# Kernel optimization log

Measured on AMD Instinct MI355X. Metric: run time of the kernel, lower is better.

The kernel has to match this reference:

```python
import jax
import jax.numpy as jnp
import numpy as np

ALPHA = 0.95
NUM_POS_FREQS = 4
CROSS_WEIGHT = 0.5
TOPK = 16
EPS = 1e-12


def _pos_enc(coords):
    # coords: [N, 4] -> [N, 4 * 2 * NUM_POS_FREQS]
    N = coords.shape[0]
    freqs = 2.0 ** jnp.arange(NUM_POS_FREQS, dtype=coords.dtype)  # [F]
    angles = coords[:, :, None] * (2.0 * jnp.pi) * freqs          # [N,4,F]
    pe = jnp.concatenate([jnp.sin(angles), jnp.cos(angles)], axis=-1)  # [N,4,2F]
    return pe.reshape(N, -1)


def _cosine_sim(x, y):
    # row-wise cosine similarity: [N,C] x [M,C] -> [N,M]
    xn = x / jnp.maximum(jnp.linalg.norm(x, axis=-1, keepdims=True), EPS)
    yn = y / jnp.maximum(jnp.linalg.norm(y, axis=-1, keepdims=True), EPS)
    return xn @ yn.T


def _sparsify_topk(A, k):
    # row-wise top-k, self-loop always kept (diag forced to max before top-k)
    N = A.shape[0]
    diag = jnp.arange(N)
    A_with_self = A.at[diag, diag].set(jnp.finfo(A.dtype).max)
    _, topk_idx = jax.lax.top_k(A_with_self, k)                   # [N,k]
    mask = jnp.zeros(A.shape, dtype=bool).at[diag[:, None], topk_idx].set(True)
    return jnp.where(mask, A, jnp.zeros((), A.dtype))


def _sym_normalize(A):
    deg = jnp.clip(A.sum(axis=-1, keepdims=True), EPS, None)      # [N,1]
    d_inv_sqrt = deg ** -0.5
    return d_inv_sqrt * A * d_inv_sqrt.T


def _build_adjacency(features, coordinates, history_features, history_coords):
    B, C = features.shape
    n, K, _ = history_features.shape
    H = n * K

    cur_feats = features
    cur_pos = _pos_enc(coordinates)
    A_cur = ALPHA * _cosine_sim(cur_feats, cur_feats) + (1.0 - ALPHA) * _cosine_sim(cur_pos, cur_pos)

    hist_feats = history_features.reshape(H, C)
    hist_pos = _pos_enc(history_coords.reshape(H, 4))
    A_hist = ALPHA * _cosine_sim(hist_feats, hist_feats) + (1.0 - ALPHA) * _cosine_sim(hist_pos, hist_pos)

    A_cross = ALPHA * _cosine_sim(cur_feats, hist_feats) + (1.0 - ALPHA) * _cosine_sim(cur_pos, hist_pos)
    A_cross = CROSS_WEIGHT * A_cross

    A = jnp.block([[A_cur, A_cross], [A_cross.T, A_hist]])        # [N,N], N=B+H
    node_feats = jnp.concatenate([cur_feats, hist_feats], axis=0)

    N = A.shape[0]
    if TOPK is not None and TOPK < N:
        A = _sparsify_topk(A, TOPK)
    A = _sym_normalize(A)
    return A[None], node_feats[None]


def setup_inputs() -> dict:
    key = jax.random.key(0)
    k1, k2, k3, k4 = jax.random.split(key, 4)
    B, C, n, K = 4096, 256, 128, 32
    return {
        "features": jax.random.normal(k1, (B, C), dtype=jnp.float32),
        "coordinates": jax.random.uniform(k2, (B, 4), dtype=jnp.float32),
        "history_features": jax.random.normal(k3, (n, K, C), dtype=jnp.float32),
        "history_coords": jax.random.uniform(k4, (n, K, 4), dtype=jnp.float32),
    }


def reference(features, coordinates, history_features, history_coords):
    adj, node_feats = _build_adjacency(features, coordinates, history_features, history_coords)
    return adj, node_feats
```

## Files before the change

### kernel.cpp

```cpp
#include <hip/hip_runtime.h>
#include <math.h>

#define B_CUR 4096
#define N_TOT 8192
#define C_F   256
#define C_TOT 288
#define KSEL  16
#define NTILE 64

typedef unsigned short u16;
typedef __attribute__((ext_vector_type(8))) short short8;
typedef __attribute__((ext_vector_type(4))) float floatx4;

__device__ inline float bf2f(u16 v) {
  union { unsigned int u; float f; } x; x.u = ((unsigned int)v) << 16; return x.f;
}
__device__ inline u16 f2bf(float f) {
  union { float f; unsigned int u; } x; x.f = f;
  unsigned int u = x.u;
  u += ((u >> 16) & 1u) + 0x7FFFu;
  return (u16)(u >> 16);
}

#define GLD_LDS16(g, l) __builtin_amdgcn_global_load_lds(                      \
    (const __attribute__((address_space(1))) unsigned int*)(g),                \
    (__attribute__((address_space(3))) unsigned int*)(l), 16, 0, 0)

__global__ __launch_bounds__(256) void k_prep(
    const float* __restrict__ feats, const float* __restrict__ hfeats,
    const float* __restrict__ coords, const float* __restrict__ hcoords,
    u16* __restrict__ Zb, float* __restrict__ out_nf) {
  int wave = threadIdx.x >> 6;
  int lane = threadIdx.x & 63;
  int row  = blockIdx.x * 4 + wave;
  const float* src = (row < B_CUR) ? (feats + (size_t)row * C_F)
                                   : (hfeats + (size_t)(row - B_CUR) * C_F);
  int c0 = lane * 4;
  float4 raw = *(const float4*)(src + c0);
  float ss = raw.x*raw.x + raw.y*raw.y + raw.z*raw.z + raw.w*raw.w;
  #pragma unroll
  for (int m = 32; m; m >>= 1) ss += __shfl_xor(ss, m, 64);
  float scale = 0.97467943448089633f / fmaxf(sqrtf(ss), 1e-12f);
  ushort4 o;
  o.x = f2bf(raw.x*scale); o.y = f2bf(raw.y*scale);
  o.z = f2bf(raw.z*scale); o.w = f2bf(raw.w*scale);
  *(ushort4*)(Zb + (size_t)row * C_TOT + c0) = o;
  *(float4*)(out_nf + (size_t)row * C_F + c0) = raw;

  const float* csrc = (row < B_CUR) ? (coords + (size_t)row * 4)
                                    : (hcoords + (size_t)(row - B_CUR) * 4);
  int d = lane >> 3, sc = (lane >> 2) & 1, f = lane & 3;
  float c = csrc[d & 3];
  float ang = c * 6.283185307179586f * (float)(1 << f);
  float pe = sc ? cosf(ang) : sinf(ang);
  float p2 = pe * pe;
  #pragma unroll
  for (int m = 16; m; m >>= 1) p2 += __shfl_xor(p2, m, 64);
  float pscale = 0.22360679774997896f / fmaxf(sqrtf(p2), 1e-12f);
  if (lane < 32) Zb[(size_t)row * C_TOT + C_F + lane] = f2bf(pe * pscale);
}

#define EP_STRIDE 136
__global__ __launch_bounds__(256) void k_gemm_mfma(const u16* __restrict__ Zb,
                                                   u16* __restrict__ adj16) {
  __shared__ __align__(16) u16 smem[2 * 128 * 96];
  u16* As = smem;
  u16* Bs = smem + 128 * 96;
  int tid  = threadIdx.x;

  int t = blockIdx.x;
  int bi = (int)floorf(((2.0f*NTILE + 1.0f) -
            sqrtf((float)((2*NTILE+1)*(2*NTILE+1)) - 8.0f*(float)t)) * 0.5f);
  if (bi < 0) bi = 0; if (bi > NTILE-1) bi = NTILE-1;
  while (bi > 0 && t < bi*NTILE - bi*(bi-1)/2) --bi;
  while (bi < NTILE-1 && t >= (bi+1)*NTILE - (bi+1)*bi/2) ++bi;
  int bj = bi + (t - (bi*NTILE - bi*(bi-1)/2));

  int wave = tid >> 6, lane = tid & 63;
  int quad = lane >> 4, l16 = lane & 15;
  int m0w  = (wave >> 1) * 64;
  int n0w  = (wave & 1) * 64;
  int i0   = bi * 128, j0 = bj * 128;

  floatx4 acc[4][4];
  #pragma unroll
  for (int a = 0; a < 4; ++a)
    #pragma unroll
    for (int b = 0; b < 4; ++b) acc[a][b] = (floatx4){0.f, 0.f, 0.f, 0.f};

  for (int kt = 0; kt < C_TOT; kt += 96) {
    #pragma unroll
    for (int it = 0; it < 6; ++it) {
      int s   = it * 256 + tid;
      int row = s / 12, seg = s % 12;
      const u16* ga = Zb + (size_t)(i0 + row) * C_TOT + kt + seg * 8;
      const u16* gb = Zb + (size_t)(j0 + row) * C_TOT + kt + seg * 8;
      GLD_LDS16(ga, As + s * 8);
      GLD_LDS16(gb, Bs + s * 8);
    }
    __builtin_amdgcn_s_waitcnt(0);
    __syncthreads();
    #pragma unroll
    for (int ks = 0; ks < 3; ++ks) {
      short8 af[4], bf[4];
      #pragma unroll
      for (int mi = 0; mi < 4; ++mi)
        af[mi] = *(const short8*)(&As[(m0w + mi*16 + l16) * 96 + ks*32 + quad*8]);
      #pragma unroll
      for (int ni = 0; ni < 4; ++ni)
        bf[ni] = *(const short8*)(&Bs[(n0w + ni*16 + l16) * 96 + ks*32 + quad*8]);
      #pragma unroll
      for (int mi = 0; mi < 4; ++mi)
        #pragma unroll
        for (int ni = 0; ni < 4; ++ni)
          acc[mi][ni] = __builtin_amdgcn_mfma_f32_16x16x32_bf16(
              af[mi], bf[ni], acc[mi][ni], 0, 0, 0);
    }
    __syncthreads();
  }

  float w = ((bi < 32) != (bj < 32)) ? 0.5f : 1.0f;

  #pragma unroll
  for (int mi = 0; mi < 4; ++mi) {
    #pragma unroll
    for (int ni = 0; ni < 4; ++ni) {
      int col = n0w + ni * 16 + l16;
      #pragma unroll
      for (int rg = 0; rg < 4; ++rg) {
        int row = m0w + mi * 16 + quad * 4 + rg;
        smem[row * EP_STRIDE + col] = f2bf(acc[mi][ni][rg] * w);
      }
    }
  }
  __syncthreads();
  #pragma unroll
  for (int it = 0; it < 8; ++it) {
    int idx = it * 256 + tid;
    int row = idx >> 4, l = idx & 15;
    uint4 v = *(const uint4*)(&smem[row * EP_STRIDE + l * 8]);
    *(uint4*)(&adj16[(size_t)(i0 + row) * 16384 + j0 + l * 8]) = v;
  }

  if (bi != bj) {
    __syncthreads();
    #pragma unroll
    for (int mi = 0; mi < 4; ++mi) {
      #pragma unroll
      for (int ni = 0; ni < 4; ++ni) {
        int col = n0w + ni * 16 + l16;
        #pragma unroll
        for (int rg = 0; rg < 4; ++rg) {
          int row = m0w + mi * 16 + quad * 4 + rg;
          smem[col * EP_STRIDE + row] = f2bf(acc[mi][ni][rg] * w);
        }
      }
    }
    __syncthreads();
    #pragma unroll
    for (int it = 0; it < 8; ++it) {
      int idx = it * 256 + tid;
      int row = idx >> 4, l = idx & 15;
      uint4 v = *(const uint4*)(&smem[row * EP_STRIDE + l * 8]);
      *(uint4*)(&adj16[(size_t)(j0 + row) * 16384 + i0 + l * 8]) = v;
    }
  }
}

__global__ __launch_bounds__(256) void k_topk(
    const u16* adj16, float* adj,
    int* __restrict__ topk_idx, float* __restrict__ topk_val,
    float* __restrict__ deg_out) {
  __shared__ unsigned int cand[64];
  __shared__ float s_diag;
  int r = blockIdx.x;
  int t = threadIdx.x;
  int wave = t >> 6, lane = t & 63;
  const u16* rowp = adj16 + (size_t)r * 16384;

  uint4 raw[4];
  #pragma unroll
  for (int j = 0; j < 4; ++j)
    raw[j] = *(const uint4*)(rowp + j * 2048 + t * 8);
  if (t == 0) s_diag = bf2f(rowp[r]);
  __syncthreads();

  {
    float* oro = adj + (size_t)r * N_TOT;
    const float4 z4 = make_float4(0.f, 0.f, 0.f, 0.f);
    #pragma unroll
    for (int kk = 0; kk < 8; ++kk)
      *(float4*)(oro + kk * 1024 + t * 4) = z4;
  }

  unsigned int keys[32];
  #pragma unroll
  for (int j = 0; j < 4; ++j) {
    int c0 = j * 2048 + t * 8;
    u16 e[8]; *(uint4*)e = raw[j];
    #pragma unroll
    for (int q = 0; q < 8; ++q) {
      int col = c0 + q;
      unsigned int b = e[q];
      unsigned int s16 = (b & 0x8000u) ? (b ^ 0xFFFFu) : (b | 0x8000u);
      unsigned int k = (s16 << 16) | (unsigned int)(8191 - col);
      if (col == r) k = 0xFFFF0000u | (unsigned int)(8191 - r);
      keys[j * 8 + q] = k;
    }
  }

  unsigned int m1 = 0, m2 = 0; int i1 = 0, i2 = 0;
  #pragma unroll
  for (int i = 0; i < 32; ++i) {
    unsigned int k = keys[i];
    if (k > m1) { m2 = m1; i2 = i1; m1 = k; i1 = i; }
    else if (k > m2) { m2 = k; i2 = i; }
  }
  unsigned int taken = 0;

  for (int it = 0; it < KSEL; ++it) {
    unsigned int wmax = m1;
    #pragma unroll
    for (int s = 32; s; s >>= 1) {
      unsigned int o = (unsigned int)__shfl_xor((int)wmax, s, 64);
      wmax = (o > wmax) ? o : wmax;
    }
    if (lane == it) cand[wave * 16 + it] = wmax;
    if (m1 == wmax && m1 != 0) {
      taken |= 1u << i1;
      if (m2 != 0) { m1 = m2; i1 = i2; m2 = 0; }
      else {
        m1 = 0; m2 = 0; i1 = 0; i2 = 0;
        #pragma unroll
        for (int i = 0; i < 32; ++i) {
          unsigned int k = (taken & (1u << i)) ? 0u : keys[i];
          if (k > m1) { m2 = m1; i2 = i1; m1 = k; i1 = i; }
          else if (k > m2) { m2 = k; i2 = i; }
        }
      }
    }
  }
  __syncthreads();

  if (wave == 0) {
    unsigned int c = cand[lane];
    unsigned int myWin = 0;
    for (int it = 0; it < KSEL; ++it) {
      unsigned int wmax = c;
      #pragma unroll
      for (int s = 32; s; s >>= 1) {
        unsigned int o = (unsigned int)__shfl_xor((int)wmax, s, 64);
        wmax = (o > wmax) ? o : wmax;
      }
      if (c == wmax) c = 0;
      if (lane == it) myWin = wmax;
    }
    float val = 0.f;
    int col = 0;
    if (lane < KSEL) {
      unsigned int p = myWin;
      col = 8191 - (int)(p & 0x1FFFu);
      unsigned int k16 = p >> 16;
      unsigned int b = (k16 & 0x8000u) ? (k16 ^ 0x8000u) : ((~k16) & 0xFFFFu);
      val = (col == r) ? s_diag : bf2f((u16)b);
      topk_idx[r * KSEL + lane] = col;
      topk_val[r * KSEL + lane] = val;
    }
    float s = (lane < KSEL) ? val : 0.f;
    #pragma unroll
    for (int m = 8; m; m >>= 1) s += __shfl_xor(s, m, 64);
    if (lane == 0) deg_out[r] = s;
  }
}

__global__ void k_scale(float* __restrict__ adj, const int* __restrict__ topk_idx,
                        const float* __restrict__ topk_val,
                        const float* __restrict__ deg) {
  int g = blockIdx.x * blockDim.x + threadIdx.x;
  if (g >= N_TOT * KSEL) return;
  int r = g >> 4, m = g & 15;
  int j = topk_idx[r * KSEL + m];
  if (j < 0) j = 0; if (j >= N_TOT) j = N_TOT - 1;
  float v = topk_val[r * KSEL + m];
  float di = 1.0f / sqrtf(fmaxf(deg[r], 1e-12f));
  float dj = 1.0f / sqrtf(fmaxf(deg[j], 1e-12f));
  adj[(size_t)r * N_TOT + j] = v * di * dj;
}

extern "C" void kernel_launch(void* const* d_in, const int* in_sizes, int n_in,
                              void* d_out, int out_size, void* d_ws, size_t ws_size,
                              hipStream_t stream) {
  const float* feats   = (const float*)d_in[0];
  const float* coords  = (const float*)d_in[1];
  const float* hfeats  = (const float*)d_in[2];
  const float* hcoords = (const float*)d_in[3];
  float* out    = (float*)d_out;
  float* adj    = out;
  u16*   adj16  = (u16*)out;
  float* out_nf = out + (size_t)N_TOT * N_TOT;

  char* ws    = (char*)d_ws;
  u16*  Zb    = (u16*)ws;
  size_t zb   = (size_t)N_TOT * C_TOT * sizeof(u16);
  zb = (zb + 255) & ~(size_t)255;
  int*   t_idx = (int*)(ws + zb);
  float* t_val = (float*)(ws + zb + (size_t)N_TOT*KSEL*sizeof(int));
  float* deg   = (float*)(ws + zb + (size_t)N_TOT*KSEL*(sizeof(int)+sizeof(float)));

  hipLaunchKernelGGL(k_prep, dim3(N_TOT/4), dim3(256), 0, stream,
                     feats, hfeats, coords, hcoords, Zb, out_nf);
  hipLaunchKernelGGL(k_gemm_mfma, dim3(NTILE*(NTILE+1)/2), dim3(256), 0, stream,
                     Zb, adj16);
  hipLaunchKernelGGL(k_topk, dim3(N_TOT), dim3(256), 0, stream,
                     adj16, adj, t_idx, t_val, deg);
  hipLaunchKernelGGL(k_scale, dim3((N_TOT*KSEL + 255)/256), dim3(256), 0, stream,
                     adj, t_idx, t_val, deg);
}
```

Baseline: 379.3 us.

## Prune top-k row reads using per-tile row maxima computed in GEMM epilogue

```diff
diff --git a/kernel.cpp b/kernel.cpp
--- a/kernel.cpp
+++ b/kernel.cpp
@@ -11,6 +11,7 @@
 typedef unsigned short u16;
 typedef __attribute__((ext_vector_type(8))) short short8;
 typedef __attribute__((ext_vector_type(4))) float floatx4;
+typedef __attribute__((ext_vector_type(4))) float f32x4;
 
 __device__ inline float bf2f(u16 v) {
   union { unsigned int u; float f; } x; x.u = ((unsigned int)v) << 16; return x.f;
@@ -36,16 +37,16 @@
   const float* src = (row < B_CUR) ? (feats + (size_t)row * C_F)
                                    : (hfeats + (size_t)(row - B_CUR) * C_F);
   int c0 = lane * 4;
-  float4 raw = *(const float4*)(src + c0);
-  float ss = raw.x*raw.x + raw.y*raw.y + raw.z*raw.z + raw.w*raw.w;
+  f32x4 raw = *(const f32x4*)(src + c0);
+  float ss = raw[0]*raw[0] + raw[1]*raw[1] + raw[2]*raw[2] + raw[3]*raw[3];
   #pragma unroll
   for (int m = 32; m; m >>= 1) ss += __shfl_xor(ss, m, 64);
   float scale = 0.97467943448089633f / fmaxf(sqrtf(ss), 1e-12f);
   ushort4 o;
-  o.x = f2bf(raw.x*scale); o.y = f2bf(raw.y*scale);
-  o.z = f2bf(raw.z*scale); o.w = f2bf(raw.w*scale);
+  o.x = f2bf(raw[0]*scale); o.y = f2bf(raw[1]*scale);
+  o.z = f2bf(raw[2]*scale); o.w = f2bf(raw[3]*scale);
   *(ushort4*)(Zb + (size_t)row * C_TOT + c0) = o;
-  *(float4*)(out_nf + (size_t)row * C_F + c0) = raw;
+  __builtin_nontemporal_store(raw, (f32x4*)(out_nf + (size_t)row * C_F + c0));
 
   const float* csrc = (row < B_CUR) ? (coords + (size_t)row * 4)
                                     : (hcoords + (size_t)(row - B_CUR) * 4);
@@ -62,7 +63,8 @@
 
 #define EP_STRIDE 136
 __global__ __launch_bounds__(256) void k_gemm_mfma(const u16* __restrict__ Zb,
-                                                   u16* __restrict__ adj16) {
+                                                   u16* __restrict__ adj16,
+                                                   u16* __restrict__ smax) {
   __shared__ __align__(16) u16 smem[2 * 128 * 96];
   u16* As = smem;
   u16* Bs = smem + 128 * 96;
@@ -134,6 +136,21 @@
     }
   }
   __syncthreads();
+  {
+    int row = tid >> 1, half = tid & 1;
+    const u16* rp = &smem[row * EP_STRIDE + half * 64];
+    float mx = -3.0e38f;
+    #pragma unroll
+    for (int q = 0; q < 8; ++q) {
+      uint4 v = *(const uint4*)(rp + q * 8);
+      const u16* e = (const u16*)&v;
+      #pragma unroll
+      for (int z = 0; z < 8; ++z) mx = fmaxf(mx, bf2f(e[z]));
+    }
+    float o2 = __shfl_xor(mx, 1, 64);
+    mx = fmaxf(mx, o2);
+    if (half == 0) smax[(size_t)(i0 + row) * 64 + bj] = f2bf(mx);
+  }
   #pragma unroll
   for (int it = 0; it < 8; ++it) {
     int idx = it * 256 + tid;
@@ -157,6 +174,21 @@
       }
     }
     __syncthreads();
+    {
+      int row = tid >> 1, half = tid & 1;
+      const u16* rp = &smem[row * EP_STRIDE + half * 64];
+      float mx = -3.0e38f;
+      #pragma unroll
+      for (int q = 0; q < 8; ++q) {
+        uint4 v = *(const uint4*)(rp + q * 8);
+        const u16* e = (const u16*)&v;
+        #pragma unroll
+        for (int z = 0; z < 8; ++z) mx = fmaxf(mx, bf2f(e[z]));
+      }
+      float o2 = __shfl_xor(mx, 1, 64);
+      mx = fmaxf(mx, o2);
+      if (half == 0) smax[(size_t)(j0 + row) * 64 + bi] = f2bf(mx);
+    }
     #pragma unroll
     for (int it = 0; it < 8; ++it) {
       int idx = it * 256 + tid;
@@ -168,42 +200,69 @@
 }
 
 __global__ __launch_bounds__(256) void k_topk(
-    const u16* adj16, float* adj,
+    const u16* adj16, float* adj, const u16* __restrict__ smax,
     int* __restrict__ topk_idx, float* __restrict__ topk_val,
     float* __restrict__ deg_out) {
   __shared__ unsigned int cand[64];
   __shared__ float s_diag;
+  __shared__ u16 s_surv[64];
   int r = blockIdx.x;
   int t = threadIdx.x;
   int wave = t >> 6, lane = t & 63;
   const u16* rowp = adj16 + (size_t)r * 16384;
 
+  if (t == 0) s_diag = bf2f(rowp[r]);
+  if (t < 64) {
+    u16 tm = smax[(size_t)r * 64 + t];
+    unsigned int s16 = (tm & 0x8000u) ? ((unsigned int)tm ^ 0xFFFFu)
+                                      : ((unsigned int)tm | 0x8000u);
+    unsigned int m = s16, T = 0;
+    for (int it = 0; it < KSEL; ++it) {
+      unsigned int wmax = m;
+      #pragma unroll
+      for (int s = 32; s; s >>= 1) {
+        unsigned int o = (unsigned int)__shfl_xor((int)wmax, s, 64);
+        wmax = (o > wmax) ? o : wmax;
+      }
+      T = wmax;
+      if (m == wmax) m = 0;
+    }
+    s_surv[t] = (s16 >= T) ? (u16)1 : (u16)0;
+  }
+  __syncthreads();
+
   uint4 raw[4];
   #pragma unroll
-  for (int j = 0; j < 4; ++j)
-    raw[j] = *(const uint4*)(rowp + j * 2048 + t * 8);
-  if (t == 0) s_diag = bf2f(rowp[r]);
+  for (int j = 0; j < 4; ++j) {
+    bool sv = s_surv[j * 16 + (t >> 4)] != 0;
+    if (sv) raw[j] = *(const uint4*)(rowp + j * 2048 + t * 8);
+    else    raw[j] = make_uint4(0u, 0u, 0u, 0u);
+  }
   __syncthreads();
 
   {
     float* oro = adj + (size_t)r * N_TOT;
-    const float4 z4 = make_float4(0.f, 0.f, 0.f, 0.f);
+    const f32x4 z4 = (f32x4){0.f, 0.f, 0.f, 0.f};
     #pragma unroll
     for (int kk = 0; kk < 8; ++kk)
-      *(float4*)(oro + kk * 1024 + t * 4) = z4;
+      __builtin_nontemporal_store(z4, (f32x4*)(oro + kk * 1024 + t * 4));
   }
 
   unsigned int keys[32];
   #pragma unroll
   for (int j = 0; j < 4; ++j) {
     int c0 = j * 2048 + t * 8;
+    bool sv = s_surv[j * 16 + (t >> 4)] != 0;
     u16 e[8]; *(uint4*)e = raw[j];
     #pragma unroll
     for (int q = 0; q < 8; ++q) {
       int col = c0 + q;
-      unsigned int b = e[q];
-      unsigned int s16 = (b & 0x8000u) ? (b ^ 0xFFFFu) : (b | 0x8000u);
-      unsigned int k = (s16 << 16) | (unsigned int)(8191 - col);
+      unsigned int k = 0;
+      if (sv) {
+        unsigned int b = e[q];
+        unsigned int s16 = (b & 0x8000u) ? (b ^ 0xFFFFu) : (b | 0x8000u);
+        k = (s16 << 16) | (unsigned int)(8191 - col);
+      }
       if (col == r) k = 0xFFFF0000u | (unsigned int)(8191 - r);
       keys[j * 8 + q] = k;
     }
@@ -306,13 +365,15 @@
   int*   t_idx = (int*)(ws + zb);
   float* t_val = (float*)(ws + zb + (size_t)N_TOT*KSEL*sizeof(int));
   float* deg   = (float*)(ws + zb + (size_t)N_TOT*KSEL*(sizeof(int)+sizeof(float)));
+  u16*   smax  = (u16*)(ws + zb + (size_t)N_TOT*KSEL*(sizeof(int)+sizeof(float))
+                                + (size_t)N_TOT*sizeof(float));
 
   hipLaunchKernelGGL(k_prep, dim3(N_TOT/4), dim3(256), 0, stream,
                      feats, hfeats, coords, hcoords, Zb, out_nf);
   hipLaunchKernelGGL(k_gemm_mfma, dim3(NTILE*(NTILE+1)/2), dim3(256), 0, stream,
-                     Zb, adj16);
+                     Zb, adj16, smax);
   hipLaunchKernelGGL(k_topk, dim3(N_TOT), dim3(256), 0, stream,
-                     adj16, adj, t_idx, t_val, deg);
+                     adj16, adj, smax, t_idx, t_val, deg);
   hipLaunchKernelGGL(k_scale, dim3((N_TOT*KSEL + 255)/256), dim3(256), 0, stream,
                      adj, t_idx, t_val, deg);
 }
```

Result: slower. 414.6 us (+9.3%).
